# Kernel optimization log

Measured on AMD Instinct MI355X. Metric: run time of the kernel, lower is better.

The kernel has to match this reference:

```python
import jax, jax.numpy as jnp
import numpy as np

NW = 6        # number of optical modes (wires)
CUT = 2       # Fock cutoff dimension
EMBED = 64    # 2**NW probabilities = embed_len
NUM_LAYERS = 2
EPS = 1e-5    # torch LayerNorm default

# ---- truncated (cutoff=2) Fock-basis gate matrices ----

def _sq(r):
    # Squeezing S(r, phi) truncated to {|0>,|1>}: diagonal, phi drops out
    # (<0|S|0> = sech(r)^0.5, <1|S|1> = sech(r)^1.5, odd/even parity kills off-diag)
    sech = 1.0 / jnp.cosh(r)
    d = jnp.stack([jnp.sqrt(sech), sech * jnp.sqrt(sech)])
    return jnp.diag(d.astype(jnp.complex64))

def _rot(phi):
    # Rotation R(phi) = diag(e^{i n phi}); also Kerr at cutoff 2 (e^{i k n^2})
    e = jnp.exp(1j * phi.astype(jnp.complex64))
    return jnp.diag(jnp.stack([jnp.ones_like(e), e]))

def _disp(r, phi):
    # Displacement D(alpha), alpha = r e^{i phi}; exact Fock elements truncated
    a = r * jnp.exp(1j * phi.astype(jnp.complex64))
    pref = jnp.exp(-0.5 * r * r)
    m = jnp.stack([jnp.stack([jnp.ones_like(a), -jnp.conj(a)]),
                   jnp.stack([a, (1.0 - r * r) * jnp.ones_like(a)])])
    return pref * m

def _bs(theta, phi):
    # Beamsplitter B = exp(theta(e^{i phi} a b+ - e^{-i phi} a+ b)), truncated.
    # Basis |n_a n_b>, index = 2*n_a + n_b. |11> -> cos(2 theta)|11> after truncation.
    c = jnp.cos(theta)
    s = jnp.sin(theta)
    ep = jnp.exp(1j * phi.astype(jnp.complex64))
    em = jnp.conj(ep)
    o = jnp.ones_like(ep)
    z = jnp.zeros_like(ep)
    return jnp.stack([
        jnp.stack([o, z, z, z]),
        jnp.stack([z, c * o, ep * s, z]),
        jnp.stack([z, -em * s, c * o, z]),
        jnp.stack([z, z, z, jnp.cos(2.0 * theta) * o]),
    ])

# ---- state-vector gate application (single sample, state shape (2,)*NW) ----

def _ap1(state, U, w):
    s = jnp.moveaxis(state, w, 0).reshape(2, -1)
    s = U @ s
    return jnp.moveaxis(s.reshape((2,) * NW), 0, w)

def _ap2(state, U, w):  # acts on wires (w, w+1)
    s = jnp.moveaxis(state, (w, w + 1), (0, 1)).reshape(4, -1)
    s = U @ s
    return jnp.moveaxis(s.reshape((2,) * NW), (0, 1), (w, w + 1))

def circuit(x, var):
    # x: (64,) features, var: (2, 50) layer weights -> (64,) probabilities
    state = jnp.zeros((2,) * NW, jnp.complex64).at[(0,) * NW].set(1.0)
    # --- data encoding ---
    for w in range(NW):
        state = _ap1(state, _sq(x[2 * w]), w)                  # x[0:12]
    for i in range(NW - 1):
        state = _ap2(state, _bs(x[12 + 2 * i], x[13 + 2 * i]), i)  # x[12:22]
    for w in range(NW):
        state = _ap1(state, _rot(x[22 + w]), w)                # x[22:28]
    for w in range(NW):
        state = _ap1(state, _disp(x[28 + 2 * w], x[29 + 2 * w]), w)  # x[28:40]
    for w in range(NW):
        state = _ap1(state, _rot(x[40 + w]), w)                # Kerr, x[40:46]
    for w in range(NW):
        state = _ap1(state, _sq(x[46 + 2 * w]), w)             # x[46:58]
    for w in range(NW):
        state = _ap1(state, _rot(x[58 + w]), w)                # x[58:64]
    # --- variational layers ---
    for l in range(NUM_LAYERS):
        v = var[l]
        for i in range(NW - 1):
            state = _ap2(state, _bs(v[2 * i], v[2 * i + 1]), i)       # v[0:10]
        for w in range(NW):
            state = _ap1(state, _rot(v[10 + w]), w)                   # v[10:16]
        for w in range(NW):
            state = _ap1(state, _sq(v[16 + w]), w)                    # v[16:22]
        for i in range(NW - 1):
            state = _ap2(state, _bs(v[22 + 2 * i], v[23 + 2 * i]), i) # v[22:32]
        for w in range(NW):
            state = _ap1(state, _rot(v[32 + w]), w)                   # v[32:38]
        for w in range(NW):
            state = _ap1(state, _disp(v[38 + w], jnp.zeros_like(v[38 + w])), w)  # v[38:44]
        for w in range(NW):
            state = _ap1(state, _rot(v[44 + w]), w)                   # Kerr, v[44:50]
    amp = state.reshape(-1)  # wire 0 is most significant, matching qml.probs
    return (jnp.abs(amp) ** 2).astype(jnp.float32)


def setup_inputs() -> dict:
    key = jax.random.key(0)
    kx, k1, k2, k3, k4, k5 = jax.random.split(key, 6)
    B, S = 32, 4096
    x = jax.random.normal(kx, (B, S, EMBED), jnp.float32)
    # WeightInitializer: passive_sd=0.1 for interferometers, active_sd=1e-4 otherwise
    int1 = 0.1 * jax.random.normal(k1, (NUM_LAYERS, 16), jnp.float32)
    sw = 1e-4 * jax.random.normal(k2, (NUM_LAYERS, NW), jnp.float32)
    int2 = 0.1 * jax.random.normal(k3, (NUM_LAYERS, 16), jnp.float32)
    dr = 1e-4 * jax.random.normal(k4, (NUM_LAYERS, NW), jnp.float32)
    kr = 1e-4 * jax.random.normal(k5, (NUM_LAYERS, NW), jnp.float32)
    var = jnp.concatenate([int1, sw, int2, dr, kr], axis=1)  # (2, 50)
    gamma = jnp.ones((EMBED,), jnp.float32)
    beta = jnp.zeros((EMBED,), jnp.float32)
    return {"x": x, "var": var, "gamma": gamma, "beta": beta}


def reference(x, var, gamma, beta):
    B, S, E = x.shape
    probs = jax.vmap(circuit, in_axes=(0, None))(x.reshape(-1, E), var)
    y = probs.reshape(B, S, E) + x  # dropout is identity in eval mode
    mu = jnp.mean(y, axis=-1, keepdims=True)
    v = jnp.var(y, axis=-1, keepdims=True)
    return (y - mu) / jnp.sqrt(v + EPS) * gamma + beta
```

## Files before the change

kernel.cpp:

```cpp
#include <hip/hip_runtime.h>
#include <hip/hip_bf16.h>
#include <math.h>

typedef _Float16 f16x8 __attribute__((ext_vector_type(8)));
typedef float f32x4 __attribute__((ext_vector_type(4)));


__device__ __forceinline__ void rot_gate(float& re, float& im, int r, int bit, float th) {
  float s, c;
  __sincosf(th, &s, &c);
  if ((r >> bit) & 1) {
    float nr = re * c - im * s;
    float ni = re * s + im * c;
    re = nr; im = ni;
  }
}

__device__ __forceinline__ void sq_gate(float& re, float& im, int r, int bit, float rr) {
  float sech = 1.0f / coshf(rr);
  float f0 = sqrtf(sech);
  float f1 = sech * f0;
  float m = ((r >> bit) & 1) ? f1 : f0;
  re *= m; im *= m;
}

__device__ __forceinline__ void disp_gate(float& re, float& im, int r, int bit, float a) {
  float pref = __expf(-0.5f * a * a);
  float pre = __shfl_xor(re, 1 << bit, 64);
  float pim = __shfl_xor(im, 1 << bit, 64);
  int b = (r >> bit) & 1;
  float A = pref * (b ? (1.0f - a * a) : 1.0f);
  float B = pref * (b ? a : -a);
  re = A * re + B * pre;
  im = A * im + B * pim;
}

__device__ __forceinline__ void bs_gate(float& re, float& im, int r, int bita, int bitb,
                                        float th, float ph) {
  float s, c;  __sincosf(th, &s, &c);
  float sp, cp; __sincosf(ph, &sp, &cp);
  float c2 = c * c - s * s;
  int na = (r >> bita) & 1;
  int nb = (r >> bitb) & 1;
  int mask = (1 << bita) | (1 << bitb);
  float pre = __shfl_xor(re, mask, 64);
  float pim = __shfl_xor(im, mask, 64);
  float A, Tr, Ti;
  if (na == nb) {
    A = na ? c2 : 1.0f; Tr = 0.0f; Ti = 0.0f;
  } else {
    A = c;
    Tr = na ? (-s * cp) : (s * cp);
    Ti = s * sp;
  }
  float nr = A * re + Tr * pre - Ti * pim;
  float ni = A * im + Tr * pim + Ti * pre;
  re = nr; im = ni;
}

__global__ __launch_bounds__(64) void build_M(const float* __restrict__ var,
                                              float2* __restrict__ M) {
  const int c = blockIdx.x;
  const int r = threadIdx.x;
  float re = (r == c) ? 1.0f : 0.0f;
  float im = 0.0f;
  for (int l = 0; l < 2; ++l) {
    const float* v = var + l * 50;
    for (int i = 0; i < 5; ++i) bs_gate(re, im, r, 5 - i, 4 - i, v[2 * i], v[2 * i + 1]);
    for (int w = 0; w < 6; ++w) rot_gate(re, im, r, 5 - w, v[10 + w]);
    for (int w = 0; w < 6; ++w) sq_gate(re, im, r, 5 - w, v[16 + w]);
    for (int i = 0; i < 5; ++i) bs_gate(re, im, r, 5 - i, 4 - i, v[22 + 2 * i], v[23 + 2 * i]);
    for (int w = 0; w < 6; ++w) rot_gate(re, im, r, 5 - w, v[32 + w]);
    for (int w = 0; w < 6; ++w) disp_gate(re, im, r, 5 - w, v[38 + w]);
    for (int w = 0; w < 6; ++w) rot_gate(re, im, r, 5 - w, v[44 + w]);
  }
  M[r * 64 + c] = make_float2(re, im);
}


__global__ __launch_bounds__(256) void pack_W(const float2* __restrict__ M,
                                              _Float16* __restrict__ Wp) {
  int tt = blockIdx.x * 256 + threadIdx.x;
  for (int idx = tt; idx < 2048; idx += 1024) {
    int lane = idx & 63;
    int kk = (idx >> 6) & 3;
    int rt = idx >> 8;
    int m = rt * 16 + (lane & 15);
    int k0 = kk * 32 + (lane >> 4) * 8;
    f16x8 h;
    #pragma unroll
    for (int j = 0; j < 8; ++j) {
      int k = k0 + j;
      float v;
      if (m < 64) {
        v = (k < 64) ? M[m * 64 + k].x : -M[m * 64 + (k - 64)].y;
      } else {
        v = (k < 64) ? M[(m - 64) * 64 + k].y : M[(m - 64) * 64 + (k - 64)].x;
      }
      h[j] = (_Float16)v;
    }
    *(f16x8*)(Wp + (size_t)idx * 8) = h;
  }
}


__global__ __launch_bounds__(256) void ff_main(const float* __restrict__ x,
                                               const float* __restrict__ gamma,
                                               const float* __restrict__ beta,
                                               const _Float16* __restrict__ Wp,
                                               float* __restrict__ out) {
  __shared__ __align__(16) _Float16 Wl[16384];
  __shared__ __align__(16) _Float16 Sl[8192];
  __shared__ float xl[64 * 65];

  const int t = threadIdx.x;
  const size_t base = (size_t)blockIdx.x * (64 * 64);

  {
    const float4* src = (const float4*)Wp;
    float4* dst = (float4*)Wl;
    #pragma unroll
    for (int i = 0; i < 8; ++i) dst[i * 256 + t] = src[i * 256 + t];
  }
  {
    const float4* xv = (const float4*)(x + base);
    #pragma unroll
    for (int i = 0; i < 4; ++i) {
      int ci = i * 256 + t;
      float4 q = xv[ci];
      int fi = ci * 4;
      int s = fi >> 6;
      int j = fi & 63;
      float* row = &xl[s * 65 + j];
      row[0] = q.x; row[1] = q.y; row[2] = q.z; row[3] = q.w;
    }
  }
  __syncthreads();

  {
    const int s = t >> 2, p = t & 3;
    const float* X = &xl[s * 65];

    float t0[6], t1r[6], t1i[6];
    #pragma unroll
    for (int w = 0; w < 6; ++w) {
      float r1  = X[2 * w];
      float rd  = X[28 + 2 * w];
      float pd  = X[29 + 2 * w];
      float kk_ = X[40 + w];
      float r2  = X[46 + 2 * w];
      float th2 = X[58 + w];
      float sech1 = 1.0f / coshf(r1);
      float sech2 = 1.0f / coshf(r2);
      float s1h = sqrtf(sech1);
      float s2h = sqrtf(sech2);
      float pref = __expf(-0.5f * rd * rd);
      float c0 = s1h * pref;
      t0[w] = c0 * s2h;
      float m1 = c0 * rd * sech2 * s2h;
      float ph = pd + kk_ + th2;
      float sp, cp;
      __sincosf(ph, &sp, &cp);
      t1r[w] = m1 * cp;
      t1i[w] = m1 * sp;
    }

    float pr, pi;
    {
      int b0 = (p >> 1) & 1, b1 = p & 1;
      float a0r = b0 ? t1r[0] : t0[0];
      float a0i = b0 ? t1i[0] : 0.0f;
      float a1r = b1 ? t1r[1] : t0[1];
      float a1i = b1 ? t1i[1] : 0.0f;
      pr = a0r * a1r - a0i * a1i;
      pi = a0r * a1i + a0i * a1r;
    }

    float tr[16], ti[16];
    tr[0] = pr; ti[0] = pi;
    #pragma unroll
    for (int st = 0; st < 4; ++st) {
      const int w = 5 - st;
      const int half = 1 << st;
      #pragma unroll
      for (int n = 0; n < half; ++n) {
        float br = tr[n], bi = ti[n];
        tr[n + half] = br * t1r[w] - bi * t1i[w];
        ti[n + half] = br * t1i[w] + bi * t1r[w];
        tr[n] = br * t0[w];
        ti[n] = bi * t0[w];
      }
    }

    const int ws_ = s >> 4, c = s & 15;
    const int kkre = p >> 1;
    #pragma unroll
    for (int j8 = 0; j8 < 2; ++j8) {
      const int q = ((p & 1) << 1) + j8;
      f16x8 hre, him;
      #pragma unroll
      for (int j = 0; j < 8; ++j) {
        hre[j] = (_Float16)tr[j8 * 8 + j];
        him[j] = (_Float16)ti[j8 * 8 + j];
      }
      *(f16x8*)&Sl[(size_t)((ws_ * 4 + kkre) * 64 + q * 16 + c) * 8] = hre;
      *(f16x8*)&Sl[(size_t)((ws_ * 4 + kkre + 2) * 64 + q * 16 + c) * 8] = him;
    }
  }
  __syncthreads();

  const int w = t >> 6;
  const int lane = t & 63;
  const int q = lane >> 4;
  const int c = lane & 15;

  f32x4 acc[8];
  #pragma unroll
  for (int rt = 0; rt < 8; ++rt) acc[rt] = (f32x4){0.0f, 0.0f, 0.0f, 0.0f};

  #pragma unroll
  for (int kk = 0; kk < 4; ++kk) {
    f16x8 b = *(const f16x8*)&Sl[(size_t)((w * 4 + kk) * 64 + lane) * 8];
    #pragma unroll
    for (int rt = 0; rt < 8; ++rt) {
      f16x8 a = *(const f16x8*)&Wl[(size_t)((rt * 4 + kk) * 64 + lane) * 8];
      acc[rt] = __builtin_amdgcn_mfma_f32_16x16x32_f16(a, b, acc[rt], 0, 0, 0);
    }
  }

  const int s = w * 16 + c;
  float y[4][4];
  float s1 = 0.0f, s2 = 0.0f;
  #pragma unroll
  for (int rt = 0; rt < 4; ++rt) {
    #pragma unroll
    for (int reg = 0; reg < 4; ++reg) {
      float re = acc[rt][reg];
      float im = acc[rt + 4][reg];
      int j = rt * 16 + q * 4 + reg;
      float yy = fmaf(re, re, im * im) + xl[s * 65 + j];
      y[rt][reg] = yy;
      s1 += yy;
      s2 += yy * yy;
    }
  }
  s1 += __shfl_xor(s1, 16, 64); s1 += __shfl_xor(s1, 32, 64);
  s2 += __shfl_xor(s2, 16, 64); s2 += __shfl_xor(s2, 32, 64);
  float mu = s1 * (1.0f / 64.0f);
  float inv = rsqrtf(fmaf(s2, 1.0f / 64.0f, -mu * mu) + 1e-5f);

  #pragma unroll
  for (int rt = 0; rt < 4; ++rt) {
    int j0 = rt * 16 + q * 4;
    float4 g = *(const float4*)(gamma + j0);
    float4 bb = *(const float4*)(beta + j0);
    float4 o;
    o.x = (y[rt][0] - mu) * inv * g.x + bb.x;
    o.y = (y[rt][1] - mu) * inv * g.y + bb.y;
    o.z = (y[rt][2] - mu) * inv * g.z + bb.z;
    o.w = (y[rt][3] - mu) * inv * g.w + bb.w;
    *(float4*)(out + base + (size_t)s * 64 + j0) = o;
  }
}

extern "C" void kernel_launch(void* const* d_in, const int* in_sizes, int n_in,
                              void* d_out, int out_size, void* d_ws, size_t ws_size,
                              hipStream_t stream) {
  const float* x     = (const float*)d_in[0];
  const float* var   = (const float*)d_in[1];
  const float* gamma = (const float*)d_in[2];
  const float* beta  = (const float*)d_in[3];
  float* out = (float*)d_out;

  float2* M = (float2*)d_ws;
  _Float16* Wp = (_Float16*)((char*)d_ws + 64 * 64 * 8);

  build_M<<<64, 64, 0, stream>>>(var, M);
  pack_W<<<4, 256, 0, stream>>>(M, Wp);

  int nsamples = in_sizes[0] / 64;
  int blocks = nsamples / 64;
  ff_main<<<blocks, 256, 0, stream>>>(x, gamma, beta, Wp, out);
}
```

Before: 123.6 us.

## Fuse matrix build and pack, read weights from global, cheaper sech

```diff
diff --git a/kernel.cpp b/kernel.cpp
--- a/kernel.cpp
+++ b/kernel.cpp
@@ -17,7 +17,8 @@
 }
 
 __device__ __forceinline__ void sq_gate(float& re, float& im, int r, int bit, float rr) {
-  float sech = 1.0f / coshf(rr);
+  float u = __expf(-fabsf(rr));
+  float sech = 2.0f * u / (1.0f + u * u);
   float f0 = sqrtf(sech);
   float f1 = sech * f0;
   float m = ((r >> bit) & 1) ? f1 : f0;
@@ -58,30 +59,33 @@
   re = nr; im = ni;
 }
 
-__global__ __launch_bounds__(64) void build_M(const float* __restrict__ var,
-                                              float2* __restrict__ M) {
-  const int c = blockIdx.x;
-  const int r = threadIdx.x;
-  float re = (r == c) ? 1.0f : 0.0f;
-  float im = 0.0f;
-  for (int l = 0; l < 2; ++l) {
-    const float* v = var + l * 50;
-    for (int i = 0; i < 5; ++i) bs_gate(re, im, r, 5 - i, 4 - i, v[2 * i], v[2 * i + 1]);
-    for (int w = 0; w < 6; ++w) rot_gate(re, im, r, 5 - w, v[10 + w]);
-    for (int w = 0; w < 6; ++w) sq_gate(re, im, r, 5 - w, v[16 + w]);
-    for (int i = 0; i < 5; ++i) bs_gate(re, im, r, 5 - i, 4 - i, v[22 + 2 * i], v[23 + 2 * i]);
-    for (int w = 0; w < 6; ++w) rot_gate(re, im, r, 5 - w, v[32 + w]);
-    for (int w = 0; w < 6; ++w) disp_gate(re, im, r, 5 - w, v[38 + w]);
-    for (int w = 0; w < 6; ++w) rot_gate(re, im, r, 5 - w, v[44 + w]);
-  }
-  M[r * 64 + c] = make_float2(re, im);
-}
-
-
-__global__ __launch_bounds__(256) void pack_W(const float2* __restrict__ M,
-                                              _Float16* __restrict__ Wp) {
-  int tt = blockIdx.x * 256 + threadIdx.x;
-  for (int idx = tt; idx < 2048; idx += 1024) {
+
+__global__ __launch_bounds__(1024) void build_pack(const float* __restrict__ var,
+                                                   _Float16* __restrict__ Wp) {
+  __shared__ float2 Msh[4096];
+  const int t = threadIdx.x;
+  const int wv = t >> 6;
+  const int r = t & 63;
+
+  for (int i = 0; i < 4; ++i) {
+    const int c = wv * 4 + i;
+    float re = (r == c) ? 1.0f : 0.0f;
+    float im = 0.0f;
+    for (int l = 0; l < 2; ++l) {
+      const float* v = var + l * 50;
+      for (int g = 0; g < 5; ++g) bs_gate(re, im, r, 5 - g, 4 - g, v[2 * g], v[2 * g + 1]);
+      for (int w = 0; w < 6; ++w) rot_gate(re, im, r, 5 - w, v[10 + w]);
+      for (int w = 0; w < 6; ++w) sq_gate(re, im, r, 5 - w, v[16 + w]);
+      for (int g = 0; g < 5; ++g) bs_gate(re, im, r, 5 - g, 4 - g, v[22 + 2 * g], v[23 + 2 * g]);
+      for (int w = 0; w < 6; ++w) rot_gate(re, im, r, 5 - w, v[32 + w]);
+      for (int w = 0; w < 6; ++w) disp_gate(re, im, r, 5 - w, v[38 + w]);
+      for (int w = 0; w < 6; ++w) rot_gate(re, im, r, 5 - w, v[44 + w]);
+    }
+    Msh[r * 64 + c] = make_float2(re, im);
+  }
+  __syncthreads();
+
+  for (int idx = t; idx < 2048; idx += 1024) {
     int lane = idx & 63;
     int kk = (idx >> 6) & 3;
     int rt = idx >> 8;
@@ -93,9 +97,9 @@
       int k = k0 + j;
       float v;
       if (m < 64) {
-        v = (k < 64) ? M[m * 64 + k].x : -M[m * 64 + (k - 64)].y;
+        v = (k < 64) ? Msh[m * 64 + k].x : -Msh[m * 64 + (k - 64)].y;
       } else {
-        v = (k < 64) ? M[(m - 64) * 64 + k].y : M[(m - 64) * 64 + (k - 64)].x;
+        v = (k < 64) ? Msh[(m - 64) * 64 + k].y : Msh[(m - 64) * 64 + (k - 64)].x;
       }
       h[j] = (_Float16)v;
     }
@@ -104,24 +108,17 @@
 }
 
 
-__global__ __launch_bounds__(256) void ff_main(const float* __restrict__ x,
-                                               const float* __restrict__ gamma,
-                                               const float* __restrict__ beta,
-                                               const _Float16* __restrict__ Wp,
-                                               float* __restrict__ out) {
-  __shared__ __align__(16) _Float16 Wl[16384];
+__global__ __launch_bounds__(256, 4) void ff_main(const float* __restrict__ x,
+                                                  const float* __restrict__ gamma,
+                                                  const float* __restrict__ beta,
+                                                  const _Float16* __restrict__ Wp,
+                                                  float* __restrict__ out) {
   __shared__ __align__(16) _Float16 Sl[8192];
   __shared__ float xl[64 * 65];
 
   const int t = threadIdx.x;
   const size_t base = (size_t)blockIdx.x * (64 * 64);
 
-  {
-    const float4* src = (const float4*)Wp;
-    float4* dst = (float4*)Wl;
-    #pragma unroll
-    for (int i = 0; i < 8; ++i) dst[i * 256 + t] = src[i * 256 + t];
-  }
   {
     const float4* xv = (const float4*)(x + base);
     #pragma unroll
@@ -150,8 +147,10 @@
       float kk_ = X[40 + w];
       float r2  = X[46 + 2 * w];
       float th2 = X[58 + w];
-      float sech1 = 1.0f / coshf(r1);
-      float sech2 = 1.0f / coshf(r2);
+      float u1 = __expf(-fabsf(r1));
+      float sech1 = 2.0f * u1 / (1.0f + u1 * u1);
+      float u2 = __expf(-fabsf(r2));
+      float sech2 = 2.0f * u2 / (1.0f + u2 * u2);
       float s1h = sqrtf(sech1);
       float s2h = sqrtf(sech2);
       float pref = __expf(-0.5f * rd * rd);
@@ -214,6 +213,8 @@
   const int q = lane >> 4;
   const int c = lane & 15;
 
+  const f16x8* Wf = (const f16x8*)Wp;
+
   f32x4 acc[8];
   #pragma unroll
   for (int rt = 0; rt < 8; ++rt) acc[rt] = (f32x4){0.0f, 0.0f, 0.0f, 0.0f};
@@ -223,7 +224,7 @@
     f16x8 b = *(const f16x8*)&Sl[(size_t)((w * 4 + kk) * 64 + lane) * 8];
     #pragma unroll
     for (int rt = 0; rt < 8; ++rt) {
-      f16x8 a = *(const f16x8*)&Wl[(size_t)((rt * 4 + kk) * 64 + lane) * 8];
+      f16x8 a = Wf[(size_t)(rt * 4 + kk) * 64 + lane];
       acc[rt] = __builtin_amdgcn_mfma_f32_16x16x32_f16(a, b, acc[rt], 0, 0, 0);
     }
   }
@@ -272,11 +273,9 @@
   const float* beta  = (const float*)d_in[3];
   float* out = (float*)d_out;
 
-  float2* M = (float2*)d_ws;
-  _Float16* Wp = (_Float16*)((char*)d_ws + 64 * 64 * 8);
-
-  build_M<<<64, 64, 0, stream>>>(var, M);
-  pack_W<<<4, 256, 0, stream>>>(M, Wp);
+  _Float16* Wp = (_Float16*)d_ws;
+
+  build_pack<<<1, 1024, 0, stream>>>(var, Wp);
 
   int nsamples = in_sizes[0] / 64;
   int blocks = nsamples / 64;
```

Measured after the change: 142.6 us. +15.3%, slower.
